# Performance work log

Measured on AMD Instinct MI355X. Metric: run time of the kernel, lower is better.

Reference implementation:

```python
import jax, jax.numpy as jnp
import numpy as np

D = 512       # d_model
H = 8         # n_heads
HD = D // H   # head_dim = 64
BS = 64       # block_size
B = 1
S = 8192
NB = S // BS  # 128 blocks
THRESH = 0.3


def setup_inputs() -> dict:
    key = jax.random.key(0)
    ks = jax.random.split(key, 6)
    sc = 0.02
    return {
        "x": jax.random.normal(ks[0], (B, S, D), jnp.float32),
        "w_qkv": (jax.random.normal(ks[1], (D, 3 * D)) * sc).astype(jnp.float32),
        "b_qkv": jnp.zeros((3 * D,), jnp.float32),
        "w_out": (jax.random.normal(ks[2], (D, D)) * sc).astype(jnp.float32),
        "b_out": jnp.zeros((D,), jnp.float32),
        "w_r1": (jax.random.normal(ks[3], (D, 128)) * sc).astype(jnp.float32),
        "b_r1": jnp.zeros((128,), jnp.float32),
        "w_r2": (jax.random.normal(ks[4], (128, 1)) * sc).astype(jnp.float32),
        "b_r2": jnp.full((1,), 0.5, jnp.float32),  # sigmoid(~0.5)>0.3 -> non-degenerate mask
    }


def reference(x, w_qkv, b_qkv, w_out, b_out, w_r1, b_r1, w_r2, b_r2):
    Bx, Sx, Dx = x.shape
    qkv = (x @ w_qkv + b_qkv).reshape(Bx, Sx, 3, H, HD)
    q = jnp.transpose(qkv[:, :, 0], (0, 2, 1, 3))  # [B,H,S,HD]
    k = jnp.transpose(qkv[:, :, 1], (0, 2, 1, 3))
    v = jnp.transpose(qkv[:, :, 2], (0, 2, 1, 3))

    # --- router: per-block importance from mean-pooled q block (d_model features) ---
    qb = q.reshape(Bx, H, NB, BS, HD)
    rep = jnp.transpose(qb.mean(axis=3), (0, 2, 1, 3)).reshape(Bx, NB, Dx)  # [B,NB,D]
    imp = jax.nn.sigmoid(jax.nn.relu(rep @ w_r1 + b_r1) @ w_r2 + b_r2)[..., 0]  # [B,NB]
    keep = (imp.mean(axis=0) >= THRESH).astype(x.dtype)  # [NB], shared across batch (torch uses batch-mean)

    kb = k.reshape(Bx, H, NB, BS, HD)
    vb = v.reshape(Bx, H, NB, BS, HD)
    tri = jnp.triu(jnp.ones((BS, BS), bool), 1)  # strict upper triangle within diagonal block
    jidx = jnp.arange(NB)
    scale = 1.0 / np.sqrt(HD)

    def step(carry, i):
        q_i = jax.lax.dynamic_slice_in_dim(q, i * BS, BS, axis=2)        # [B,H,BSq,HD]
        s = jnp.einsum('bhqd,bhjkd->bhqjk', q_i, kb) * scale             # [B,H,BSq,NB,BSk]
        causal = (jidx == i)[None, :, None] & tri[:, None, :]            # [BSq,NB,BSk]
        s = jnp.where(causal[None, None], -jnp.inf, s)
        p = jax.nn.softmax(s, axis=-1)                                   # softmax PER key-block (as in torch loop)
        wj = keep * keep[i]                                              # block pair gate [NB]
        o = jnp.einsum('bhqjk,j,bhjkd->bhqd', p, wj, vb)                 # sum of gated per-block contributions
        return carry, o

    _, outs = jax.lax.scan(step, None, jnp.arange(NB))                   # [NB,B,H,BSq,HD]
    attn = jnp.transpose(outs, (1, 2, 0, 3, 4)).reshape(Bx, H, Sx, HD)
    attn = jnp.transpose(attn, (0, 2, 1, 3)).reshape(Bx, Sx, Dx)
    return attn @ w_out + b_out
```

## Files before the change

kernel.cpp:

```cpp
#include <hip/hip_runtime.h>

typedef unsigned short u16;
typedef unsigned int u32;
typedef __attribute__((ext_vector_type(8))) short short8;
typedef __attribute__((ext_vector_type(4))) short short4v;
typedef __attribute__((ext_vector_type(4))) float f32x4;
typedef __attribute__((ext_vector_type(4))) float float4v;
typedef __attribute__((ext_vector_type(2))) u32 u32x2;
typedef __attribute__((ext_vector_type(4))) u32 u32x4;

#define S_LEN 8192
#define NHEAD 8
#define NBLK  128
#define SCALE_C 0.18033688011112042f

__device__ __forceinline__ u16 f2b(float f) {
    union { float f; unsigned u; } v; v.f = f;
    unsigned r = v.u + 0x7FFFu + ((v.u >> 16) & 1u);
    return (u16)(r >> 16);
}
__device__ __forceinline__ float b2f(u16 b) {
    union { float f; unsigned u; } v; v.u = ((unsigned)b) << 16; return v.f;
}
__device__ __forceinline__ u32 cvt_pk_bf16(float lo, float hi) {
    u32 r;
    asm("v_cvt_pk_bf16_f32 %0, %1, %2" : "=v"(r) : "v"(lo), "v"(hi));
    return r;
}
__device__ __forceinline__ void pl16swap(u32& a, u32& b) {
    u32x2 r = __builtin_amdgcn_permlane16_swap(a, b, false, false);
    a = r[0]; b = r[1];
}
__device__ __forceinline__ void pl32swap(u32& a, u32& b) {
    u32x2 r = __builtin_amdgcn_permlane32_swap(a, b, false, false);
    a = r[0]; b = r[1];
}
__device__ __forceinline__ int swz(int row, int colByte) {
    return row * 128 + (colByte ^ ((row & 7) << 4));
}
__device__ __forceinline__ void gload_lds(const void* g, void* l) {
    __builtin_amdgcn_global_load_lds(
        (const __attribute__((address_space(1))) void*)g,
        (__attribute__((address_space(3))) void*)l, 16, 0, 0);
}

__global__ __launch_bounds__(256) void cvt_x_kernel(const float* __restrict__ x, u16* __restrict__ xb) {
    int idx = blockIdx.x * 256 + threadIdx.x;
    float4v v = *((const float4v*)x + idx);
    short4v o;
    #pragma unroll
    for (int r = 0; r < 4; ++r) o[r] = (short)f2b(v[r]);
    *((short4v*)xb + idx) = o;
}

__global__ __launch_bounds__(256) void cvt_T_kernel(const float* __restrict__ w, u16* __restrict__ wt, int C) {
    int idx = blockIdx.x * 256 + threadIdx.x;
    int r = idx & 511, cc = idx >> 9;
    wt[idx] = f2b(w[(size_t)r * C + cc]);
}

__global__ __launch_bounds__(256) void sum4_kernel(const u16* __restrict__ a0, const u16* __restrict__ a1,
                                                   const u16* __restrict__ a2, const u16* __restrict__ a3,
                                                   int n, u16* __restrict__ outb) {
    int idx = blockIdx.x * 256 + threadIdx.x;
    short8 v0 = ((const short8*)a0)[idx];
    short8 v1 = ((const short8*)a1)[idx];
    float s[8];
    #pragma unroll
    for (int e = 0; e < 8; ++e) s[e] = b2f((u16)v0[e]) + b2f((u16)v1[e]);
    if (n == 4) {
        short8 v2 = ((const short8*)a2)[idx];
        short8 v3 = ((const short8*)a3)[idx];
        #pragma unroll
        for (int e = 0; e < 8; ++e) s[e] += b2f((u16)v2[e]) + b2f((u16)v3[e]);
    }
    short8 o;
    #pragma unroll
    for (int e = 0; e < 8; ++e) o[e] = (short)f2b(s[e]);
    ((short8*)outb)[idx] = o;
}

__device__ __forceinline__ void gemm128_core(const u16* __restrict__ A,
                                             const u16* __restrict__ Bt,
                                             int m0, int n0, char* As, char* Bs,
                                             f32x4 acc[4][4]) {
    const int tid = threadIdx.x;
    const int lane = tid & 63, wid = tid >> 6;
    const int q16 = lane >> 4, l16 = lane & 15;
    const int wm = wid >> 1, wn = wid & 1;
    #pragma unroll 1
    for (int kt = 0; kt < 8; ++kt) {
        const int k0 = kt * 64;
        __syncthreads();
        #pragma unroll
        for (int p = 0; p < 4; ++p) {
            int c = tid + p * 256;
            int row = c >> 3, colp = (c & 7) ^ (row & 7);
            gload_lds(A  + (size_t)(m0 + row) * 512 + k0 + colp * 8, As + (size_t)(wid * 64 + p * 256) * 16);
            gload_lds(Bt + (size_t)(n0 + row) * 512 + k0 + colp * 8, Bs + (size_t)(wid * 64 + p * 256) * 16);
        }
        __syncthreads();
        #pragma unroll
        for (int kk = 0; kk < 2; ++kk) {
            short8 a[4], b[4];
            #pragma unroll
            for (int t = 0; t < 4; ++t) {
                int arow = wm * 64 + t * 16 + l16;
                a[t] = *(const short8*)(As + swz(arow, kk * 64 + q16 * 16));
                int brow = wn * 64 + t * 16 + l16;
                b[t] = *(const short8*)(Bs + swz(brow, kk * 64 + q16 * 16));
            }
            #pragma unroll
            for (int mt = 0; mt < 4; ++mt)
                #pragma unroll
                for (int nt = 0; nt < 4; ++nt)
                    acc[mt][nt] = __builtin_amdgcn_mfma_f32_16x16x32_bf16(a[mt], b[nt], acc[mt][nt], 0, 0, 0);
        }
    }
}

__global__ __launch_bounds__(256) void qkv_gemm(const u16* __restrict__ xb, const u16* __restrict__ wqkvT,
                                                const float* __restrict__ bqkv,
                                                u16* __restrict__ qb, u16* __restrict__ kf, u16* __restrict__ vf) {
    __shared__ char smem[32768];
    f32x4 acc[4][4];
    #pragma unroll
    for (int a = 0; a < 4; ++a)
        #pragma unroll
        for (int b = 0; b < 4; ++b) acc[a][b] = (f32x4){0.f, 0.f, 0.f, 0.f};
    const int m0 = blockIdx.x * 128, n0 = blockIdx.y * 128;
    gemm128_core(xb, wqkvT, m0, n0, smem, smem + 16384, acc);

    const int lane = threadIdx.x & 63, wid = threadIdx.x >> 6;
    const int q16 = lane >> 4, l16 = lane & 15;
    const int wm = wid >> 1, wn = wid & 1;
    #pragma unroll
    for (int mt = 0; mt < 4; ++mt) {
        #pragma unroll
        for (int nt = 0; nt < 4; ++nt) {
            int n = n0 + wn * 64 + nt * 16 + l16;
            float bias = bqkv[n];
            int t = n >> 9, h = (n >> 6) & 7, d = n & 63;
            int sb = m0 + wm * 64 + mt * 16 + q16 * 4;
            f32x4 v = acc[mt][nt];
            if (t == 0) {
                #pragma unroll
                for (int r = 0; r < 4; ++r)
                    qb[(size_t)(h * S_LEN + sb + r) * 64 + d] = f2b((v[r] + bias) * SCALE_C);
            } else if (t == 1) {
                int j = sb >> 6, key = sb & 63;
                int n0k = key >> 4, c = d >> 5, q16k = (d >> 3) & 3, e = d & 7;
                int ub = (n0k * 2 + c) * 64 + q16k * 16 + (key & 15);
                u16* base = kf + (size_t)h * 524288 + (size_t)j * 4096 + e;
                #pragma unroll
                for (int r = 0; r < 4; ++r)
                    base[(ub + r) * 8] = f2b(v[r] + bias);
            } else {
                int j = sb >> 6, key = sb & 63;
                int dt = d >> 4, c = key >> 5, q16v = (key >> 3) & 3, e0 = key & 7;
                int u = (dt * 2 + c) * 64 + q16v * 16 + (d & 15);
                short4v pk;
                #pragma unroll
                for (int r = 0; r < 4; ++r) pk[r] = (short)f2b(v[r] + bias);
                *(short4v*)(vf + (size_t)h * 524288 + (size_t)j * 4096 + u * 8 + e0) = pk;
            }
        }
    }
}

__global__ __launch_bounds__(256) void out_gemm(const u16* __restrict__ a0, const u16* __restrict__ wotT,
                                                const float* __restrict__ bout, float* __restrict__ out) {
    __shared__ char smem[32768];
    f32x4 acc[4][4];
    #pragma unroll
    for (int a = 0; a < 4; ++a)
        #pragma unroll
        for (int b = 0; b < 4; ++b) acc[a][b] = (f32x4){0.f, 0.f, 0.f, 0.f};
    const int m0 = blockIdx.x * 128, n0 = blockIdx.y * 128;
    gemm128_core(a0, wotT, m0, n0, smem, smem + 16384, acc);

    const int lane = threadIdx.x & 63, wid = threadIdx.x >> 6;
    const int q16 = lane >> 4, l16 = lane & 15;
    const int wm = wid >> 1, wn = wid & 1;
    #pragma unroll
    for (int mt = 0; mt < 4; ++mt) {
        #pragma unroll
        for (int nt = 0; nt < 4; ++nt) {
            int n = n0 + wn * 64 + nt * 16 + l16;
            float bias = bout[n];
            int sb = m0 + wm * 64 + mt * 16 + q16 * 4;
            #pragma unroll
            for (int r = 0; r < 4; ++r)
                out[(size_t)(sb + r) * 512 + n] = acc[mt][nt][r] + bias;
        }
    }
}

__global__ __launch_bounds__(256) void router_kernel(const u16* __restrict__ qb,
                                                     const float* __restrict__ w_r1, const float* __restrict__ b_r1,
                                                     const float* __restrict__ w_r2, const float* __restrict__ b_r2,
                                                     float* __restrict__ keepf) {
    const int nb = blockIdx.x, tid = threadIdx.x;
    __shared__ float rep[512];
    __shared__ float h1[128];
    for (int dim = tid; dim < 512; dim += 256) {
        int h = dim >> 6, d = dim & 63;
        const u16* p = qb + (size_t)(h * S_LEN + nb * 64) * 64 + d;
        float s = 0.f;
        #pragma unroll 4
        for (int t = 0; t < 64; ++t) s += b2f(p[t * 64]);
        rep[dim] = s * (0.015625f / SCALE_C);
    }
    __syncthreads();
    if (tid < 128) {
        float a = b_r1[tid];
        for (int k = 0; k < 512; ++k) a += rep[k] * w_r1[k * 128 + tid];
        h1[tid] = fmaxf(a, 0.f);
    }
    __syncthreads();
    if (tid < 64) {
        float v = h1[tid] * w_r2[tid] + h1[tid + 64] * w_r2[tid + 64];
        #pragma unroll
        for (int off = 32; off; off >>= 1) v += __shfl_down(v, off);
        if (tid == 0) {
            float z = v + b_r2[0];
            keepf[nb] = (z >= -0.84729786f) ? 1.0f : 0.0f;
        }
    }
}

__global__ __launch_bounds__(256, 5) void attn_kernel(const u16* __restrict__ qb, const u16* __restrict__ kf,
                                                      const u16* __restrict__ vf, const float* __restrict__ keepf,
                                                      u16* __restrict__ a0, u16* __restrict__ a1,
                                                      u16* __restrict__ a2, u16* __restrict__ a3, int nj) {
    const int i = blockIdx.x, h = blockIdx.y, jh = blockIdx.z;
    const int j0 = jh * nj;
    u16* __restrict__ att = (jh == 0) ? a0 : (jh == 1) ? a1 : (jh == 2) ? a2 : a3;
    const int tid = threadIdx.x, lane = tid & 63, wid = tid >> 6;
    const int q16 = lane >> 4, l16 = lane & 15;
    __shared__ char smem[32768];

    short8 bq[2][2];
    #pragma unroll
    for (int qh = 0; qh < 2; ++qh) {
        const u16* qrow = qb + (size_t)(h * S_LEN + i * 128 + wid * 32 + qh * 16 + l16) * 64;
        bq[qh][0] = *(const short8*)(qrow + q16 * 8);
        bq[qh][1] = *(const short8*)(qrow + 32 + q16 * 8);
    }
    const int kq = i * 2 + (wid >> 1);
    const float keep_i = keepf[kq];
    const int qloc = (wid & 1) * 32 + l16;

    f32x4 o[2][4];
    #pragma unroll
    for (int qh = 0; qh < 2; ++qh)
        #pragma unroll
        for (int t = 0; t < 4; ++t) o[qh][t] = (f32x4){0.f, 0.f, 0.f, 0.f};

    const u16* kf_h = kf + (size_t)h * 524288;
    const u16* vf_h = vf + (size_t)h * 524288;
    const int lb = lane * 16;
    const int stoff = (wid * 128 + lane) * 8;
    const int ldw = wid * 2048;

    {
        const size_t b = (size_t)j0 * 4096;
        gload_lds(kf_h + b + stoff,       smem + ldw);
        gload_lds(kf_h + b + stoff + 512, smem + ldw + 1024);
        gload_lds(vf_h + b + stoff,       smem + 8192 + ldw);
        gload_lds(vf_h + b + stoff + 512, smem + 8192 + ldw + 1024);
    }
    __syncthreads();

    for (int jj = 0; jj < nj; ++jj) {
        const int j = j0 + jj;
        char* Kc = smem + ((jj & 1) << 14);
        char* Vc = Kc + 8192;
        if (jj < nj - 1) {
            char* Kn = smem + (((jj + 1) & 1) << 14);
            const size_t b = (size_t)(j + 1) * 4096;
            gload_lds(kf_h + b + stoff,       Kn + ldw);
            gload_lds(kf_h + b + stoff + 512, Kn + ldw + 1024);
            gload_lds(vf_h + b + stoff,       Kn + 8192 + ldw);
            gload_lds(vf_h + b + stoff + 512, Kn + 8192 + ldw + 1024);
        }
        const float gj = keep_i * keepf[j];

        f32x4 s4[2][4];
        __builtin_amdgcn_s_setprio(1);
        #pragma unroll
        for (int n0 = 0; n0 < 4; ++n0) {
            short8 ka0 = *(const short8*)(Kc + n0 * 2048 + lb);
            short8 ka1 = *(const short8*)(Kc + n0 * 2048 + 1024 + lb);
            #pragma unroll
            for (int qh = 0; qh < 2; ++qh) {
                f32x4 a = (f32x4){0.f, 0.f, 0.f, 0.f};
                a = __builtin_amdgcn_mfma_f32_16x16x32_bf16(ka0, bq[qh][0], a, 0, 0, 0);
                a = __builtin_amdgcn_mfma_f32_16x16x32_bf16(ka1, bq[qh][1], a, 0, 0, 0);
                s4[qh][n0] = a;
            }
        }
        __builtin_amdgcn_s_setprio(0);

        short8 pb[2][2];
        #pragma unroll
        for (int qh = 0; qh < 2; ++qh) {
            float pv[4][4];
            #pragma unroll
            for (int n0 = 0; n0 < 4; ++n0)
                #pragma unroll
                for (int r = 0; r < 4; ++r)
                    pv[n0][r] = __builtin_amdgcn_exp2f(s4[qh][n0][r]);
            if (j == kq) {
                const int qthis = qloc + qh * 16;
                #pragma unroll
                for (int n0 = 0; n0 < 4; ++n0)
                    #pragma unroll
                    for (int r = 0; r < 4; ++r)
                        if (n0 * 16 + q16 * 4 + r > qthis) pv[n0][r] = 0.f;
            }
            float sum = 0.f;
            #pragma unroll
            for (int n0 = 0; n0 < 4; ++n0)
                sum += (pv[n0][0] + pv[n0][1]) + (pv[n0][2] + pv[n0][3]);
            {
                u32 sa = __builtin_bit_cast(u32, sum), sb = sa;
                pl16swap(sa, sb);
                sum = __builtin_bit_cast(float, sa) + __builtin_bit_cast(float, sb);
                u32 sc = __builtin_bit_cast(u32, sum), sd = sc;
                pl32swap(sc, sd);
                sum = __builtin_bit_cast(float, sc) + __builtin_bit_cast(float, sd);
            }
            const float rinv = gj * __builtin_amdgcn_rcpf(sum);
            u32 dw[4][2];
            #pragma unroll
            for (int n0 = 0; n0 < 4; ++n0) {
                dw[n0][0] = cvt_pk_bf16(pv[n0][0] * rinv, pv[n0][1] * rinv);
                dw[n0][1] = cvt_pk_bf16(pv[n0][2] * rinv, pv[n0][3] * rinv);
            }
            #pragma unroll
            for (int kk = 0; kk < 2; ++kk) {
                u32 c0 = dw[2 * kk][0], d0 = dw[2 * kk + 1][0];
                pl32swap(c0, d0);
                pl16swap(c0, d0);
                u32 c1 = dw[2 * kk][1], d1 = dw[2 * kk + 1][1];
                pl32swap(c1, d1);
                pl16swap(c1, d1);
                u32x4 wv;
                wv[0] = c0; wv[1] = c1; wv[2] = d0; wv[3] = d1;
                pb[qh][kk] = __builtin_bit_cast(short8, wv);
            }
        }

        __builtin_amdgcn_s_setprio(1);
        #pragma unroll
        for (int dt = 0; dt < 4; ++dt) {
            short8 va0 = *(const short8*)(Vc + dt * 2048 + lb);
            short8 va1 = *(const short8*)(Vc + dt * 2048 + 1024 + lb);
            #pragma unroll
            for (int qh = 0; qh < 2; ++qh) {
                o[qh][dt] = __builtin_amdgcn_mfma_f32_16x16x32_bf16(va0, pb[qh][0], o[qh][dt], 0, 0, 0);
                o[qh][dt] = __builtin_amdgcn_mfma_f32_16x16x32_bf16(va1, pb[qh][1], o[qh][dt], 0, 0, 0);
            }
        }
        __builtin_amdgcn_s_setprio(0);

        __syncthreads();
    }

    #pragma unroll
    for (int qh = 0; qh < 2; ++qh) {
        u16* obase = att + (size_t)(i * 128 + wid * 32 + qh * 16 + l16) * 512 + h * 64 + q16 * 4;
        #pragma unroll
        for (int dt = 0; dt < 4; ++dt) {
            u32x2 st;
            st[0] = cvt_pk_bf16(o[qh][dt][0], o[qh][dt][1]);
            st[1] = cvt_pk_bf16(o[qh][dt][2], o[qh][dt][3]);
            *(u32x2*)(obase + dt * 16) = st;
        }
    }
}

static const size_t OFF_WQKVT = 0;
static const size_t OFF_WOTT  = (size_t)2u << 20;
static const size_t OFF_KEEP  = ((size_t)2u << 20) + (512u << 10);
static const size_t OFF_QB    = (size_t)3u << 20;
static const size_t OFF_KF    = (size_t)11u << 20;
static const size_t OFF_VF    = (size_t)19u << 20;
static const size_t OFF_XB    = (size_t)27u << 20;
static const size_t OFF_P0    = (size_t)35u << 20;
static const size_t OFF_P1    = (size_t)43u << 20;
static const size_t OFF_P2    = (size_t)51u << 20;

extern "C" void kernel_launch(void* const* d_in, const int* in_sizes, int n_in,
                              void* d_out, int out_size, void* d_ws, size_t ws_size,
                              hipStream_t stream) {
    const float* x     = (const float*)d_in[0];
    const float* w_qkv = (const float*)d_in[1];
    const float* b_qkv = (const float*)d_in[2];
    const float* w_out = (const float*)d_in[3];
    const float* b_out = (const float*)d_in[4];
    const float* w_r1  = (const float*)d_in[5];
    const float* b_r1  = (const float*)d_in[6];
    const float* w_r2  = (const float*)d_in[7];
    const float* b_r2  = (const float*)d_in[8];
    float* out = (float*)d_out;
    char* ws = (char*)d_ws;
    u16* wqkvT  = (u16*)(ws + OFF_WQKVT);
    u16* wotT   = (u16*)(ws + OFF_WOTT);
    float* keepf = (float*)(ws + OFF_KEEP);
    u16* qb     = (u16*)(ws + OFF_QB);
    u16* kf     = (u16*)(ws + OFF_KF);
    u16* vf     = (u16*)(ws + OFF_VF);
    u16* xb     = (u16*)(ws + OFF_XB);
    u16* attnb  = (u16*)(ws + OFF_QB);

    const bool big = ws_size >= ((size_t)59u << 20) + 4096;
    const int njh = big ? 4 : 2;
    const int nj  = NBLK / njh;
    u16* a0 = (u16*)(ws + OFF_P0);
    u16* a1 = big ? (u16*)(ws + OFF_P1) : (u16*)(ws + OFF_XB);
    u16* a2 = big ? (u16*)(ws + OFF_P2) : a0;
    u16* a3 = big ? (u16*)(ws + OFF_XB) : a0;

    cvt_x_kernel<<<4096, 256, 0, stream>>>(x, xb);
    cvt_T_kernel<<<3072, 256, 0, stream>>>(w_qkv, wqkvT, 1536);
    cvt_T_kernel<<<1024, 256, 0, stream>>>(w_out, wotT, 512);
    qkv_gemm<<<dim3(64, 12), 256, 0, stream>>>(xb, wqkvT, b_qkv, qb, kf, vf);
    router_kernel<<<128, 256, 0, stream>>>(qb, w_r1, b_r1, w_r2, b_r2, keepf);
    attn_kernel<<<dim3(64, 8, njh), 256, 0, stream>>>(qb, kf, vf, keepf, a0, a1, a2, a3, nj);
    sum4_kernel<<<2048, 256, 0, stream>>>(a0, a1, a2, a3, njh, attnb);
    out_gemm<<<dim3(64, 4), 256, 0, stream>>>(attnb, wotT, b_out, out);
}
```

Measured before the change: 250.5 us.

## Triple-buffer K/V tiles in LDS with prefetch depth two

The attention loop moves from double to triple buffering of K/V tiles in shared memory and prefetches two tiles ahead. The end-of-iteration __syncthreads is replaced by a partial vmcnt wait plus a barrier at the top of each iteration, so a load can stay in flight across a full compute step. The cost is 48KB of LDS instead of 32KB, with the occupancy hint lowered from 5 to 3 blocks per CU, which reduces latency hiding across waves. The vmcnt(4) count relies on each stage issuing exactly four loads per thread; on the last iteration no new stage is issued, so the wait may not fully cover the final tile.

```diff
diff --git a/kernel.cpp b/kernel.cpp
--- a/kernel.cpp
+++ b/kernel.cpp
@@ -229,7 +229,7 @@
     }
 }
 
-__global__ __launch_bounds__(256, 5) void attn_kernel(const u16* __restrict__ qb, const u16* __restrict__ kf,
+__global__ __launch_bounds__(256, 3) void attn_kernel(const u16* __restrict__ qb, const u16* __restrict__ kf,
                                                       const u16* __restrict__ vf, const float* __restrict__ keepf,
                                                       u16* __restrict__ a0, u16* __restrict__ a1,
                                                       u16* __restrict__ a2, u16* __restrict__ a3, int nj) {
@@ -238,7 +238,7 @@
     u16* __restrict__ att = (jh == 0) ? a0 : (jh == 1) ? a1 : (jh == 2) ? a2 : a3;
     const int tid = threadIdx.x, lane = tid & 63, wid = tid >> 6;
     const int q16 = lane >> 4, l16 = lane & 15;
-    __shared__ char smem[32768];
+    __shared__ char smem[49152];
 
     short8 bq[2][2];
     #pragma unroll
@@ -263,27 +263,26 @@
     const int stoff = (wid * 128 + lane) * 8;
     const int ldw = wid * 2048;
 
-    {
-        const size_t b = (size_t)j0 * 4096;
-        gload_lds(kf_h + b + stoff,       smem + ldw);
-        gload_lds(kf_h + b + stoff + 512, smem + ldw + 1024);
-        gload_lds(vf_h + b + stoff,       smem + 8192 + ldw);
-        gload_lds(vf_h + b + stoff + 512, smem + 8192 + ldw + 1024);
-    }
-    __syncthreads();
+    auto stage = [&](int jt, char* dst) {
+        const size_t b = (size_t)jt * 4096;
+        gload_lds(kf_h + b + stoff,       dst + ldw);
+        gload_lds(kf_h + b + stoff + 512, dst + ldw + 1024);
+        gload_lds(vf_h + b + stoff,       dst + 8192 + ldw);
+        gload_lds(vf_h + b + stoff + 512, dst + 8192 + ldw + 1024);
+    };
+
+    stage(j0, smem);
+    stage(j0 + 1, smem + 16384);
 
     for (int jj = 0; jj < nj; ++jj) {
+        asm volatile("s_waitcnt vmcnt(4)" ::: "memory");
+        __builtin_amdgcn_s_barrier();
+        __builtin_amdgcn_sched_barrier(0);
+        if (jj + 2 < nj) stage(j0 + jj + 2, smem + ((jj + 2) % 3) * 16384);
+
         const int j = j0 + jj;
-        char* Kc = smem + ((jj & 1) << 14);
+        char* Kc = smem + (jj % 3) * 16384;
         char* Vc = Kc + 8192;
-        if (jj < nj - 1) {
-            char* Kn = smem + (((jj + 1) & 1) << 14);
-            const size_t b = (size_t)(j + 1) * 4096;
-            gload_lds(kf_h + b + stoff,       Kn + ldw);
-            gload_lds(kf_h + b + stoff + 512, Kn + ldw + 1024);
-            gload_lds(vf_h + b + stoff,       Kn + 8192 + ldw);
-            gload_lds(vf_h + b + stoff + 512, Kn + 8192 + ldw + 1024);
-        }
         const float gj = keep_i * keepf[j];
 
         f32x4 s4[2][4];
@@ -364,8 +363,6 @@
             }
         }
         __builtin_amdgcn_s_setprio(0);
-
-        __syncthreads();
     }
 
     #pragma unroll
```

After: 244.3 us. -2.5%, faster.
